# Performance work log

Hardware: AMD Instinct MI355X
Metric: run time of the kernel (lower is better)

The kernel has to match this reference:

```python
import jax, jax.numpy as jnp
import numpy as np

B, N, G, C = 4, 4000, 64, 91
H, W = 800.0, 1333.0
FG_THRESH, BG_THRESH = 0.5, 0.5
SCORE_THRESH, NMS_THRESH = 0.05, 0.5
DET_PER_IMG = 100
PRE_NMS_TOPK = 2048   # candidates entering NMS per image
MIN_SIZE = 0.01
BBOX_XFORM_CLIP = float(np.log(1000.0 / 16.0))
WX, WY, WW, WH = 10.0, 10.0, 5.0, 5.0  # bbox_reg_weights


def _rand_boxes(key, shape):
    k1, k2 = jax.random.split(key)
    xy = jax.random.uniform(k1, shape[:-1] + (2,)) * jnp.array([W * 0.8, H * 0.8], jnp.float32)
    wh = jax.random.uniform(k2, shape[:-1] + (2,)) * jnp.array([W * 0.2, H * 0.2], jnp.float32) + 2.0
    return jnp.concatenate([xy, xy + wh], axis=-1)


def setup_inputs():
    key = jax.random.key(0)
    ks = jax.random.split(key, 5)
    proposals = _rand_boxes(ks[0], (B, N, 4))
    gt_boxes = _rand_boxes(ks[1], (B, G, 4))
    gt_labels = jax.random.randint(ks[2], (B, G), 1, C)
    class_logits = jax.random.normal(ks[3], (B, N, C), dtype=jnp.float32)
    box_regression = jax.random.normal(ks[4], (B, N, C * 4), dtype=jnp.float32) * 0.1
    return {"proposals": proposals, "gt_boxes": gt_boxes, "gt_labels": gt_labels,
            "class_logits": class_logits, "box_regression": box_regression}


def box_iou(a, b):
    # a [A,4], b [B,4] -> [A,B]
    area_a = (a[:, 2] - a[:, 0]) * (a[:, 3] - a[:, 1])
    area_b = (b[:, 2] - b[:, 0]) * (b[:, 3] - b[:, 1])
    lt = jnp.maximum(a[:, None, :2], b[None, :, :2])
    rb = jnp.minimum(a[:, None, 2:], b[None, :, 2:])
    wh = jnp.clip(rb - lt, 0.0)
    inter = wh[..., 0] * wh[..., 1]
    return inter / (area_a[:, None] + area_b[None, :] - inter)


def encode(gt, prop):
    # BoxCoder.encode with weights (10,10,5,5)
    pw = prop[:, 2] - prop[:, 0]; ph = prop[:, 3] - prop[:, 1]
    px = prop[:, 0] + 0.5 * pw;  py = prop[:, 1] + 0.5 * ph
    gw = gt[:, 2] - gt[:, 0];    gh = gt[:, 3] - gt[:, 1]
    gx = gt[:, 0] + 0.5 * gw;    gy = gt[:, 1] + 0.5 * gh
    return jnp.stack([WX * (gx - px) / pw, WY * (gy - py) / ph,
                      WW * jnp.log(gw / pw), WH * jnp.log(gh / ph)], axis=1)


def decode(deltas, boxes):
    # deltas [N,C,4], boxes [N,4] -> [N,C,4]
    pw = boxes[:, 2] - boxes[:, 0]; ph = boxes[:, 3] - boxes[:, 1]
    px = boxes[:, 0] + 0.5 * pw;    py = boxes[:, 1] + 0.5 * ph
    dx = deltas[..., 0] / WX; dy = deltas[..., 1] / WY
    dw = jnp.minimum(deltas[..., 2] / WW, BBOX_XFORM_CLIP)
    dh = jnp.minimum(deltas[..., 3] / WH, BBOX_XFORM_CLIP)
    cx = dx * pw[:, None] + px[:, None]; cy = dy * ph[:, None] + py[:, None]
    w = jnp.exp(dw) * pw[:, None];       h = jnp.exp(dh) * ph[:, None]
    return jnp.stack([cx - 0.5 * w, cy - 0.5 * h, cx + 0.5 * w, cy + 0.5 * h], axis=-1)


def _image_fwd(prop, gt_b, gt_l, logits, regr):
    # --- assign_targets_to_proposals (with add_gt_proposals) ---
    props_all = jnp.concatenate([prop, gt_b], axis=0)          # [N+G,4]
    iou = box_iou(gt_b, props_all)                             # [G,N+G]
    matched_vals = iou.max(axis=0)
    matches = iou.argmax(axis=0)
    lbl = jnp.where(matched_vals >= FG_THRESH, gt_l[matches],
                    jnp.where(matched_vals < BG_THRESH, 0, -1))
    reg_targets = encode(gt_b[matches], props_all)             # [N+G,4]

    # --- postprocess_detections: decode + softmax + per-class NMS ---
    deltas = regr.reshape(N, C, 4)
    pb = decode(deltas, prop)                                  # [N,C,4]
    pb = jnp.stack([jnp.clip(pb[..., 0], 0.0, W), jnp.clip(pb[..., 1], 0.0, H),
                    jnp.clip(pb[..., 2], 0.0, W), jnp.clip(pb[..., 3], 0.0, H)], axis=-1)
    scores = jax.nn.softmax(logits, axis=-1)                   # [N,C]
    boxes_f = pb[:, 1:].reshape(-1, 4)                         # drop background class
    scores_f = scores[:, 1:].reshape(-1)
    labels_f = jnp.broadcast_to(jnp.arange(1, C), (N, C - 1)).reshape(-1)
    wf = boxes_f[:, 2] - boxes_f[:, 0]; hf = boxes_f[:, 3] - boxes_f[:, 1]
    valid = (scores_f > SCORE_THRESH) & (wf >= MIN_SIZE) & (hf >= MIN_SIZE)
    masked = jnp.where(valid, scores_f, -1.0)
    top_vals, top_idx = jax.lax.top_k(masked, PRE_NMS_TOPK)    # score-sorted candidates
    cb = boxes_f[top_idx]; cl = labels_f[top_idx]; cs = scores_f[top_idx]
    cv = top_vals > 0.0
    # batched_nms via per-class coordinate offset
    off = cl.astype(cb.dtype) * (max(W, H) + 1.0)
    ob = cb + off[:, None]
    iou_c = box_iou(ob, ob)                                    # [M,M]
    order = jnp.arange(PRE_NMS_TOPK)

    def body(i, keep):
        sup = keep[i] & (iou_c[i] > NMS_THRESH) & (order > i)
        return keep & ~sup

    keep = jax.lax.fori_loop(0, PRE_NMS_TOPK, body, cv)
    rank = jnp.cumsum(keep) - 1
    out_pos = jnp.where(keep & (rank < DET_PER_IMG), rank, DET_PER_IMG)  # OOB -> drop
    det_b = jnp.zeros((DET_PER_IMG, 4), cb.dtype).at[out_pos].set(cb, mode='drop')
    det_s = jnp.zeros((DET_PER_IMG,), cs.dtype).at[out_pos].set(cs, mode='drop')
    det_l = jnp.zeros((DET_PER_IMG,), cl.dtype).at[out_pos].set(cl, mode='drop')
    det = jnp.concatenate([det_b, det_s[:, None]], axis=-1)    # [K,5]
    return det, reg_targets, lbl, det_l


def reference(proposals, gt_boxes, gt_labels, class_logits, box_regression):
    return jax.vmap(_image_fwd)(proposals, gt_boxes, gt_labels, class_logits, box_regression)
```

## Files before the change

### kernel.cpp

```cpp
#include <hip/hip_runtime.h>
#include <cstdint>
#include <cstddef>

#define Bn   4
#define Nn   4000
#define Gn   64
#define Cn   91
#define FGC  90
#define NSEG 64
#define CAPSEG 256
#define CAPC (NSEG*CAPSEG)
#define SELCAP 4096
#define MSEL 2048
#define DETK 100

__device__ __constant__ float kW = 1333.0f;
__device__ __constant__ float kH = 800.0f;
#define XCLIP 4.135166556742356f
#define OFFMUL 1334.0f

#define NB 9216
#define SBIAS 0x3D400000u

typedef __attribute__((ext_vector_type(2))) unsigned long long u64x2;

#define OUT_DET  0
#define OUT_REG  (Bn*DETK*5)
#define OUT_LBL  (OUT_REG + Bn*(Nn+Gn)*4)
#define OUT_DETL (OUT_LBL + Bn*(Nn+Gn))

#define ZERO_N16 (148736/16)

__device__ __forceinline__ void decode_box(float4 p, float4 d,
                                           float& bx1, float& by1, float& bx2, float& by2) {
    float pw = p.z - p.x, ph = p.w - p.y;
    float px = p.x + 0.5f * pw, py = p.y + 0.5f * ph;
    float dx = d.x / 10.0f, dy = d.y / 10.0f;
    float dw = fminf(d.z / 5.0f, XCLIP), dh = fminf(d.w / 5.0f, XCLIP);
    float cx = dx * pw + px, cy = dy * ph + py;
    float w = expf(dw) * pw, h = expf(dh) * ph;
    bx1 = fminf(fmaxf(cx - 0.5f * w, 0.0f), kW);
    by1 = fminf(fmaxf(cy - 0.5f * h, 0.0f), kH);
    bx2 = fminf(fmaxf(cx + 0.5f * w, 0.0f), kW);
    by2 = fminf(fmaxf(cy + 0.5f * h, 0.0f), kH);
}

__device__ __forceinline__ unsigned score_bucket(unsigned sb) {
    unsigned h = (sb - SBIAS) >> 12;
    return h > (NB - 1) ? (NB - 1) : h;
}

__global__ __launch_bounds__(256) void zero_k(uint4* __restrict__ p) {
    int i = blockIdx.x * 256 + threadIdx.x;
    if (i < ZERO_N16) p[i] = make_uint4(0, 0, 0, 0);
}

__global__ __launch_bounds__(256) void fused_cand_k(const float* __restrict__ logits,
                                                    const float* __restrict__ regr,
                                                    const float* __restrict__ props,
                                                    unsigned long long* __restrict__ keys,
                                                    unsigned int* __restrict__ cnt,
                                                    unsigned int* __restrict__ hist) {
    int wave = threadIdx.x >> 6, lane = threadIdx.x & 63;
    int blk = blockIdx.x;
    int rowbase = blk * 16 + wave * 4;
    int b = blk / 250;
    int nbase = rowbase - b * Nn;
    bool has1 = (lane + 64) < Cn;
    const float* z = logits + (size_t)rowbase * Cn;
    float v0[4], v1[4], m[4], e[4];
    #pragma unroll
    for (int r = 0; r < 4; ++r) {
        v0[r] = z[r * Cn + lane];
        v1[r] = has1 ? z[r * Cn + lane + 64] : -INFINITY;
        m[r] = fmaxf(v0[r], v1[r]);
    }
    #pragma unroll
    for (int o = 32; o; o >>= 1) {
        #pragma unroll
        for (int r = 0; r < 4; ++r) m[r] = fmaxf(m[r], __shfl_xor(m[r], o));
    }
    #pragma unroll
    for (int r = 0; r < 4; ++r)
        e[r] = expf(v0[r] - m[r]) + (has1 ? expf(v1[r] - m[r]) : 0.0f);
    #pragma unroll
    for (int o = 32; o; o >>= 1) {
        #pragma unroll
        for (int r = 0; r < 4; ++r) e[r] += __shfl_xor(e[r], o);
    }
    unsigned long long keyA[4], keyB[4];
    bool vA[4], vB[4];
    #pragma unroll
    for (int r = 0; r < 4; ++r) {
        float s0 = expf(v0[r] - m[r]) / e[r];
        float s1 = has1 ? (expf(v1[r] - m[r]) / e[r]) : 0.0f;
        vA[r] = (lane >= 1) && (s0 > 0.05f);
        vB[r] = has1 && (s1 > 0.05f);
        keyA[r] = 0; keyB[r] = 0;
        float4 p = make_float4(0.f, 0.f, 0.f, 0.f);
        if (vA[r] || vB[r]) p = ((const float4*)props)[rowbase + r];
        if (vA[r]) {
            int c = lane;
            float4 d = ((const float4*)regr)[(size_t)(rowbase + r) * Cn + c];
            float bx1, by1, bx2, by2;
            decode_box(p, d, bx1, by1, bx2, by2);
            vA[r] = (bx2 - bx1 >= 0.01f) && (by2 - by1 >= 0.01f);
            unsigned idx = (unsigned)((nbase + r) * FGC + c - 1);
            keyA[r] = ((unsigned long long)__float_as_uint(s0) << 32) | (unsigned long long)(~idx);
            if (vA[r]) atomicAdd(&hist[b * NB + score_bucket(__float_as_uint(s0))], 1u);
        }
        if (vB[r]) {
            int c = lane + 64;
            float4 d = ((const float4*)regr)[(size_t)(rowbase + r) * Cn + c];
            float bx1, by1, bx2, by2;
            decode_box(p, d, bx1, by1, bx2, by2);
            vB[r] = (bx2 - bx1 >= 0.01f) && (by2 - by1 >= 0.01f);
            unsigned idx = (unsigned)((nbase + r) * FGC + c - 1);
            keyB[r] = ((unsigned long long)__float_as_uint(s1) << 32) | (unsigned long long)(~idx);
            if (vB[r]) atomicAdd(&hist[b * NB + score_bucket(__float_as_uint(s1))], 1u);
        }
    }
    unsigned long long mk[8];
    #pragma unroll
    for (int r = 0; r < 4; ++r) { mk[2*r] = __ballot(vA[r]); mk[2*r+1] = __ballot(vB[r]); }
    unsigned tot = 0, pre[8];
    #pragma unroll
    for (int q = 0; q < 8; ++q) { pre[q] = tot; tot += (unsigned)__popcll(mk[q]); }
    if (tot) {
        int seg = b * NSEG + (blk & (NSEG - 1));
        unsigned base = 0;
        if (lane == 0) base = atomicAdd(&cnt[seg], tot);
        base = __shfl(base, 0);
        unsigned long long lmask = (lane == 63) ? (~0ull >> 1) : ((1ull << lane) - 1);
        size_t segbase = (size_t)seg * CAPSEG;
        #pragma unroll
        for (int r = 0; r < 4; ++r) {
            if (vA[r]) {
                unsigned pos = base + pre[2*r] + (unsigned)__popcll(mk[2*r] & lmask);
                if (pos < CAPSEG) keys[segbase + pos] = keyA[r];
            }
            if (vB[r]) {
                unsigned pos = base + pre[2*r+1] + (unsigned)__popcll(mk[2*r+1] & lmask);
                if (pos < CAPSEG) keys[segbase + pos] = keyB[r];
            }
        }
    }
}

__global__ __launch_bounds__(256) void compact_k(const unsigned long long* __restrict__ keys,
                                                 const unsigned int* __restrict__ cnt,
                                                 const unsigned int* __restrict__ hist,
                                                 unsigned long long* __restrict__ sel,
                                                 unsigned int* __restrict__ cnt2) {
    int b = blockIdx.x >> 4, blk = blockIdx.x & 15;
    int tid = threadIdx.x, lane = tid & 63, wv = tid >> 6;
    __shared__ unsigned wtot[4], wt2[4], sscnt[NSEG];
    __shared__ unsigned sT, sbase;

    const uint4* h4 = (const uint4*)(hist + b * NB);
    unsigned hc[36]; unsigned s = 0;
    #pragma unroll
    for (int q = 0; q < 9; ++q) {
        uint4 t4 = h4[tid * 9 + q];
        hc[q*4+0] = t4.x; hc[q*4+1] = t4.y; hc[q*4+2] = t4.z; hc[q*4+3] = t4.w;
        s += t4.x + t4.y + t4.z + t4.w;
    }
    unsigned x = s;
    #pragma unroll
    for (int o = 1; o < 64; o <<= 1) { unsigned v = __shfl_down(x, o); if (lane + o < 64) x += v; }
    if (lane == 0) wtot[wv] = x;
    if (tid < NSEG) { unsigned c = cnt[b * NSEG + tid]; sscnt[tid] = c > CAPSEG ? CAPSEG : c; }
    __syncthreads();
    unsigned above = 0, total = 0;
    #pragma unroll
    for (int i2 = 0; i2 < 4; ++i2) { unsigned w2 = wtot[i2]; total += w2; if (i2 > wv) above += w2; }
    unsigned K2 = total < MSEL ? total : MSEL;
    if (K2 == 0) return;
    unsigned run = (x - s) + above;
    #pragma unroll
    for (int q = 35; q >= 0; --q) {
        unsigned c = hc[q], lo = run;
        run += c;
        if (lo < K2 && K2 <= run) sT = (unsigned)(tid * 36 + q);
    }
    __syncthreads();
    unsigned T = sT;

    unsigned long long k0 = 0, k1 = 0, k2 = 0, k3 = 0;
    bool v0 = false, v1 = false, v2 = false, v3 = false;
    {
        int g = blk * 1024 + 0 * 256 + tid; unsigned seg = g >> 8, ss = g & 255;
        if (ss < sscnt[seg]) { unsigned long long k = keys[(size_t)b * CAPC + g];
            if (score_bucket((unsigned)(k >> 32)) >= T) { k0 = k; v0 = true; } }
    }
    {
        int g = blk * 1024 + 1 * 256 + tid; unsigned seg = g >> 8, ss = g & 255;
        if (ss < sscnt[seg]) { unsigned long long k = keys[(size_t)b * CAPC + g];
            if (score_bucket((unsigned)(k >> 32)) >= T) { k1 = k; v1 = true; } }
    }
    {
        int g = blk * 1024 + 2 * 256 + tid; unsigned seg = g >> 8, ss = g & 255;
        if (ss < sscnt[seg]) { unsigned long long k = keys[(size_t)b * CAPC + g];
            if (score_bucket((unsigned)(k >> 32)) >= T) { k2 = k; v2 = true; } }
    }
    {
        int g = blk * 1024 + 3 * 256 + tid; unsigned seg = g >> 8, ss = g & 255;
        if (ss < sscnt[seg]) { unsigned long long k = keys[(size_t)b * CAPC + g];
            if (score_bucket((unsigned)(k >> 32)) >= T) { k3 = k; v3 = true; } }
    }
    unsigned c2 = (unsigned)v0 + (unsigned)v1 + (unsigned)v2 + (unsigned)v3;
    unsigned inc = c2;
    #pragma unroll
    for (int o = 1; o < 64; o <<= 1) { unsigned v = __shfl_up(inc, o); if (lane >= o) inc += v; }
    unsigned excl = inc - c2;
    if (lane == 63) wt2[wv] = inc;
    __syncthreads();
    if (tid == 0) {
        unsigned tot = wt2[0] + wt2[1] + wt2[2] + wt2[3];
        sbase = tot ? atomicAdd(&cnt2[b], tot) : 0u;
    }
    __syncthreads();
    unsigned pos = sbase + excl;
    #pragma unroll
    for (int i2 = 0; i2 < 4; ++i2) if (i2 < wv) pos += wt2[i2];
    unsigned long long* selb = sel + (size_t)b * SELCAP;
    unsigned q0 = pos, q1 = q0 + v0, q2 = q1 + v1, q3 = q2 + v2;
    if (v0 && q0 < SELCAP) selb[q0] = k0;
    if (v1 && q1 < SELCAP) selb[q1] = k1;
    if (v2 && q2 < SELCAP) selb[q2] = k2;
    if (v3 && q3 < SELCAP) selb[q3] = k3;
}

__global__ __launch_bounds__(256) void rank_k(const unsigned long long* __restrict__ sel,
                                              const unsigned int* __restrict__ cnt2,
                                              unsigned long long* __restrict__ selkeys) {
    int b = blockIdx.x >> 6, blk = blockIdx.x & 63;
    unsigned n2 = cnt2[b]; if (n2 > SELCAP) n2 = SELCAP;
    if ((unsigned)(blk * 64) >= n2) return;
    int lane = threadIdx.x & 63, wv = threadIdx.x >> 6;
    int sub = blk * 64 + lane;
    __shared__ __align__(16) unsigned long long skk[SELCAP + 2];
    __shared__ unsigned pc[4][64];
    unsigned n2p = (n2 + 1) & ~1u;
    const unsigned long long* selb = sel + (size_t)b * SELCAP;
    for (unsigned s2 = threadIdx.x; s2 < n2p; s2 += 256)
        skk[s2] = (s2 < n2) ? selb[s2] : 0ull;
    __syncthreads();
    unsigned long long mk = (sub < (int)n2) ? skk[sub] : ~0ull;
    bool act = (sub < (int)n2) && ((mk >> 32) != 0ull);
    unsigned pairs = n2p >> 1;
    unsigned Q = (pairs + 3) >> 2;
    unsigned jb = wv * Q, je = jb + Q; if (je > pairs) je = pairs;
    const u64x2* sk2 = (const u64x2*)skk;
    unsigned cntg = 0;
    for (unsigned j = jb; j < je; ++j) {
        u64x2 kk = sk2[j];
        cntg += (unsigned)(kk.x > mk) + (unsigned)(kk.y > mk);
    }
    pc[wv][lane] = cntg;
    __syncthreads();
    if (wv == 0) {
        unsigned rank = pc[0][lane] + pc[1][lane] + pc[2][lane] + pc[3][lane];
        if (act && rank < MSEL) selkeys[(size_t)b * MSEL + rank] = mk;
    }
}

__global__ __launch_bounds__(256) void select_k(const unsigned long long* __restrict__ selkeys,
                                                const unsigned int* __restrict__ cnt2,
                                                const float* __restrict__ props,
                                                const float* __restrict__ regr,
                                                float* __restrict__ cb, float* __restrict__ ob,
                                                float* __restrict__ sc, int* __restrict__ lab,
                                                unsigned long long* __restrict__ cvw) {
    int t = blockIdx.x * 256 + threadIdx.x;
    if (t >= Bn * MSEL) return;
    int b = t >> 11;
    unsigned n2 = cnt2[b]; if (n2 > SELCAP) n2 = SELCAP;
    unsigned validN = n2 < MSEL ? n2 : MSEL;
    unsigned slotrank = (unsigned)(t & (MSEL - 1));
    unsigned long long key = (slotrank < validN) ? selkeys[t] : 0ull;
    float bx1 = 0, by1 = 0, bx2 = 0, by2 = 0, score = 0;
    int c = 0; unsigned valid = 0;
    if ((key >> 32) != 0ull) {
        valid = 1;
        unsigned idx = ~(unsigned)key;
        int n = idx / FGC, cm1 = idx - n * FGC;
        c = cm1 + 1;
        score = __uint_as_float((unsigned)(key >> 32));
        int row = b * Nn + n;
        float4 p = ((const float4*)props)[row];
        float4 d = ((const float4*)regr)[(size_t)row * Cn + c];
        decode_box(p, d, bx1, by1, bx2, by2);
    }
    float off = (float)c * OFFMUL;
    cb[t * 4 + 0] = bx1; cb[t * 4 + 1] = by1; cb[t * 4 + 2] = bx2; cb[t * 4 + 3] = by2;
    ob[t * 4 + 0] = bx1 + off; ob[t * 4 + 1] = by1 + off;
    ob[t * 4 + 2] = bx2 + off; ob[t * 4 + 3] = by2 + off;
    sc[t] = score; lab[t] = c;
    unsigned long long bw = __ballot(valid != 0u);
    if ((t & 63) == 0) cvw[t >> 6] = bw;
}

__global__ __launch_bounds__(256) void nmsmat_k(const float* __restrict__ ob,
                                                unsigned long long* __restrict__ M) {
    int blk = blockIdx.x;
    int b = blk >> 8, rc = (blk >> 5) & 7, w = blk & 31;
    int i = rc * 256 + threadIdx.x;
    size_t mi = ((size_t)b * MSEL + i) * 32 + w;
    if (w * 64 + 63 <= rc * 256) {
        M[mi] = 0ull;
        return;
    }
    __shared__ float4 sj[64];
    const float4* obf4 = (const float4*)(ob + (size_t)b * MSEL * 4);
    if (threadIdx.x < 64) sj[threadIdx.x] = obf4[w * 64 + threadIdx.x];
    __syncthreads();
    float4 bi = obf4[i];
    float areai = (bi.z - bi.x) * (bi.w - bi.y);
    unsigned long long bits = 0ull;
    #pragma unroll 16
    for (int tt = 0; tt < 64; ++tt) {
        int j = w * 64 + tt;
        float4 bj = sj[tt];
        float xx1 = fmaxf(bi.x, bj.x), yy1 = fmaxf(bi.y, bj.y);
        float xx2 = fminf(bi.z, bj.z), yy2 = fminf(bi.w, bj.w);
        float iw = fmaxf(xx2 - xx1, 0.0f), ih = fmaxf(yy2 - yy1, 0.0f);
        float inter = iw * ih;
        float areaj = (bj.z - bj.x) * (bj.w - bj.y);
        float iou = inter / (areai + areaj - inter);
        if ((iou > 0.5f) && (j > i)) bits |= (1ull << tt);
    }
    M[mi] = bits;
}

__global__ __launch_bounds__(64) void scan_k(const unsigned long long* __restrict__ M,
                                             const unsigned long long* __restrict__ cvw,
                                             const float* __restrict__ cb,
                                             const float* __restrict__ sc,
                                             const int* __restrict__ lab,
                                             float* __restrict__ out) {
    int b = blockIdx.x, lane = threadIdx.x;
    const bool ld = lane < 32;
    unsigned long long keep = ld ? cvw[b * 32 + lane] : 0ull;
    unsigned kLo = (unsigned)keep, kHi = (unsigned)(keep >> 32);
    __shared__ int keptIdx[DETK];
    const unsigned long long* Mb = M + (size_t)b * MSEL * 32;
    int kcount = 0;
    unsigned long long Abuf[16], Bbuf[16];
    #pragma unroll
    for (int k = 0; k < 16; ++k) Abuf[k] = ld ? Mb[(size_t)k * 32 + lane] : 0ull;
    for (int g = 0; g < 128; g += 2) {
        #pragma unroll
        for (int k = 0; k < 16; ++k)
            Bbuf[k] = ld ? Mb[(size_t)((g + 1) * 16 + k) * 32 + lane] : 0ull;
        {
            int base = g * 16;
            int rl = base >> 6, sh = base & 31;
            unsigned half = (base >> 5) & 1;
            #pragma unroll
            for (int k = 0; k < 16; ++k) {
                unsigned kw = half ? kHi : kLo;
                unsigned bitv = (__builtin_amdgcn_readlane(kw, rl) >> (sh + k)) & 1u;
                if (bitv) {
                    unsigned long long m = Abuf[k];
                    kLo &= ~(unsigned)m; kHi &= ~(unsigned)(m >> 32);
                    if (kcount < DETK && lane == 0) keptIdx[kcount] = base + k;
                    ++kcount;
                }
            }
        }
        if (kcount >= DETK) break;
        if (g + 2 < 128) {
            #pragma unroll
            for (int k = 0; k < 16; ++k)
                Abuf[k] = ld ? Mb[(size_t)((g + 2) * 16 + k) * 32 + lane] : 0ull;
        }
        {
            int base = (g + 1) * 16;
            int rl = base >> 6, sh = base & 31;
            unsigned half = (base >> 5) & 1;
            #pragma unroll
            for (int k = 0; k < 16; ++k) {
                unsigned kw = half ? kHi : kLo;
                unsigned bitv = (__builtin_amdgcn_readlane(kw, rl) >> (sh + k)) & 1u;
                if (bitv) {
                    unsigned long long m = Bbuf[k];
                    kLo &= ~(unsigned)m; kHi &= ~(unsigned)(m >> 32);
                    if (kcount < DETK && lane == 0) keptIdx[kcount] = base + k;
                    ++kcount;
                }
            }
        }
        if (kcount >= DETK) break;
    }
    __syncthreads();
    int kept100 = kcount < DETK ? kcount : DETK;
    for (int r = lane; r < kept100; r += 64) {
        int i = keptIdx[r];
        int slot = b * MSEL + i;
        float* dr = out + OUT_DET + ((size_t)b * DETK + r) * 5;
        dr[0] = cb[slot * 4 + 0]; dr[1] = cb[slot * 4 + 1];
        dr[2] = cb[slot * 4 + 2]; dr[3] = cb[slot * 4 + 3];
        dr[4] = sc[slot];
        out[OUT_DETL + b * DETK + r] = (float)lab[slot];
    }
    for (int r = kept100 + lane; r < DETK; r += 64) {
        float* dr = out + OUT_DET + ((size_t)b * DETK + r) * 5;
        dr[0] = dr[1] = dr[2] = dr[3] = dr[4] = 0.0f;
        out[OUT_DETL + b * DETK + r] = 0.0f;
    }
}

__global__ __launch_bounds__(256) void assign_k(const float* __restrict__ props,
                                                const float* __restrict__ gtb,
                                                const int* __restrict__ gtl,
                                                float* __restrict__ out) {
    __shared__ float4 sg[Gn];
    int b = blockIdx.y;
    int p = blockIdx.x * 256 + threadIdx.x;
    if (threadIdx.x < Gn) sg[threadIdx.x] = ((const float4*)(gtb + (size_t)b * Gn * 4))[threadIdx.x];
    __syncthreads();
    if (p >= Nn + Gn) return;
    float4 pb = (p < Nn) ? ((const float4*)(props + (size_t)b * Nn * 4))[p] : sg[p - Nn];
    float areap = (pb.z - pb.x) * (pb.w - pb.y);
    float best = -1.0f; int bi = 0;
    #pragma unroll 4
    for (int g = 0; g < Gn; ++g) {
        float4 gb = sg[g];
        float xx1 = fmaxf(gb.x, pb.x), yy1 = fmaxf(gb.y, pb.y);
        float xx2 = fminf(gb.z, pb.z), yy2 = fminf(gb.w, pb.w);
        float iw = fmaxf(xx2 - xx1, 0.0f), ih = fmaxf(yy2 - yy1, 0.0f);
        float inter = iw * ih;
        float areag = (gb.z - gb.x) * (gb.w - gb.y);
        float iou = inter / (areag + areap - inter);
        if (iou > best) { best = iou; bi = g; }
    }
    float4 gb = sg[bi];
    float pw = pb.z - pb.x, ph = pb.w - pb.y;
    float px = pb.x + 0.5f * pw, py = pb.y + 0.5f * ph;
    float gw = gb.z - gb.x, gh = gb.w - gb.y;
    float gx = gb.x + 0.5f * gw, gy = gb.y + 0.5f * gh;
    float* rr = out + OUT_REG + ((size_t)b * (Nn + Gn) + p) * 4;
    rr[0] = 10.0f * (gx - px) / pw;
    rr[1] = 10.0f * (gy - py) / ph;
    rr[2] = 5.0f * logf(gw / pw);
    rr[3] = 5.0f * logf(gh / ph);
    out[OUT_LBL + (size_t)b * (Nn + Gn) + p] = (best >= 0.5f) ? (float)gtl[b * Gn + bi] : 0.0f;
}

extern "C" void kernel_launch(void* const* d_in, const int* in_sizes, int n_in,
                              void* d_out, int out_size, void* d_ws, size_t ws_size,
                              hipStream_t stream) {
    const float* props  = (const float*)d_in[0];
    const float* gtb    = (const float*)d_in[1];
    const int*   gtl    = (const int*)d_in[2];
    const float* logits = (const float*)d_in[3];
    const float* regr   = (const float*)d_in[4];
    float* out = (float*)d_out;

    char* w = (char*)d_ws;
    unsigned int* cnt           = (unsigned int*)(w + 0);
    unsigned int* cnt2          = (unsigned int*)(w + 1024);
    unsigned int* hist          = (unsigned int*)(w + 1280);
    unsigned long long* sel     = (unsigned long long*)(w + 148736);
    unsigned long long* selkeys = (unsigned long long*)(w + 279808);
    unsigned long long* keys    = (unsigned long long*)(w + 345344);
    float* cb                   = (float*)(w + 869632);
    float* ob                   = (float*)(w + 1000704);
    float* sc                   = (float*)(w + 1131776);
    int* lab                    = (int*)(w + 1164544);
    unsigned long long* cvw     = (unsigned long long*)(w + 1197312);
    unsigned long long* M       = (unsigned long long*)(w + 1198336);
    (void)ws_size; (void)in_sizes; (void)n_in; (void)out_size;

    zero_k<<<(ZERO_N16 + 255) / 256, 256, 0, stream>>>((uint4*)w);
    fused_cand_k<<<Bn * Nn / 16, 256, 0, stream>>>(logits, regr, props, keys, cnt, hist);
    compact_k<<<Bn * 16, 256, 0, stream>>>(keys, cnt, hist, sel, cnt2);
    rank_k<<<Bn * 64, 256, 0, stream>>>(sel, cnt2, selkeys);
    select_k<<<(Bn * MSEL) / 256, 256, 0, stream>>>(selkeys, cnt2, props, regr, cb, ob, sc, lab, cvw);
    nmsmat_k<<<Bn * 256, 256, 0, stream>>>(ob, M);
    scan_k<<<Bn, 64, 0, stream>>>(M, cvw, cb, sc, lab, out);
    assign_k<<<dim3((Nn + Gn + 255) / 256, Bn), 256, 0, stream>>>(props, gtb, gtl, out);
}
```

Baseline: 87.77 us.

## Restructure candidate pipeline: per-block slots, shared-memory histogram, fused rank-select

Each candidate block now holds 32 rows and owns a fixed key slot range. Its count goes to a shared-memory counter that is written out at the end, so the separate zeroing kernel is no longer needed. The global atomic score histogram moves into compact_k, now one block per image, which builds the histogram in shared memory from the stored keys. The rank and select kernels are fused so decode happens right at the ranked position. The valid-bit array is dropped because scan_k derives the keep mask from the selected count. Two launches go away, but compaction now runs on only four blocks and loops serially over 20000 slots each.

Result: slower. 112.0 us (+27.6%).

```diff
diff --git a/kernel.cpp b/kernel.cpp
--- a/kernel.cpp
+++ b/kernel.cpp
@@ -7,9 +7,11 @@
 #define Gn   64
 #define Cn   91
 #define FGC  90
-#define NSEG 64
-#define CAPSEG 256
-#define CAPC (NSEG*CAPSEG)
+#define RPW  8
+#define BLKROWS 32
+#define NBLKI 125
+#define CAPSEG 160
+#define SLOTSI (NBLKI*CAPSEG)
 #define SELCAP 4096
 #define MSEL 2048
 #define DETK 100
@@ -28,8 +30,6 @@
 #define OUT_REG  (Bn*DETK*5)
 #define OUT_LBL  (OUT_REG + Bn*(Nn+Gn)*4)
 #define OUT_DETL (OUT_LBL + Bn*(Nn+Gn))
-
-#define ZERO_N16 (148736/16)
 
 __device__ __forceinline__ void decode_box(float4 p, float4 d,
                                            float& bx1, float& by1, float& bx2, float& by2) {
@@ -50,27 +50,23 @@
     return h > (NB - 1) ? (NB - 1) : h;
 }
 
-__global__ __launch_bounds__(256) void zero_k(uint4* __restrict__ p) {
-    int i = blockIdx.x * 256 + threadIdx.x;
-    if (i < ZERO_N16) p[i] = make_uint4(0, 0, 0, 0);
-}
-
 __global__ __launch_bounds__(256) void fused_cand_k(const float* __restrict__ logits,
                                                     const float* __restrict__ regr,
                                                     const float* __restrict__ props,
                                                     unsigned long long* __restrict__ keys,
-                                                    unsigned int* __restrict__ cnt,
-                                                    unsigned int* __restrict__ hist) {
+                                                    unsigned int* __restrict__ cnt) {
+    __shared__ unsigned lcnt;
     int wave = threadIdx.x >> 6, lane = threadIdx.x & 63;
     int blk = blockIdx.x;
-    int rowbase = blk * 16 + wave * 4;
-    int b = blk / 250;
+    if (threadIdx.x == 0) lcnt = 0;
+    int rowbase = blk * BLKROWS + wave * RPW;
+    int b = blk / NBLKI;
     int nbase = rowbase - b * Nn;
     bool has1 = (lane + 64) < Cn;
     const float* z = logits + (size_t)rowbase * Cn;
-    float v0[4], v1[4], m[4], e[4];
-    #pragma unroll
-    for (int r = 0; r < 4; ++r) {
+    float v0[RPW], v1[RPW], m[RPW], e[RPW], t0[RPW], t1[RPW];
+    #pragma unroll
+    for (int r = 0; r < RPW; ++r) {
         v0[r] = z[r * Cn + lane];
         v1[r] = has1 ? z[r * Cn + lane + 64] : -INFINITY;
         m[r] = fmaxf(v0[r], v1[r]);
@@ -78,22 +74,25 @@
     #pragma unroll
     for (int o = 32; o; o >>= 1) {
         #pragma unroll
-        for (int r = 0; r < 4; ++r) m[r] = fmaxf(m[r], __shfl_xor(m[r], o));
-    }
-    #pragma unroll
-    for (int r = 0; r < 4; ++r)
-        e[r] = expf(v0[r] - m[r]) + (has1 ? expf(v1[r] - m[r]) : 0.0f);
+        for (int r = 0; r < RPW; ++r) m[r] = fmaxf(m[r], __shfl_xor(m[r], o));
+    }
+    #pragma unroll
+    for (int r = 0; r < RPW; ++r) {
+        t0[r] = expf(v0[r] - m[r]);
+        t1[r] = has1 ? expf(v1[r] - m[r]) : 0.0f;
+        e[r] = t0[r] + t1[r];
+    }
     #pragma unroll
     for (int o = 32; o; o >>= 1) {
         #pragma unroll
-        for (int r = 0; r < 4; ++r) e[r] += __shfl_xor(e[r], o);
-    }
-    unsigned long long keyA[4], keyB[4];
-    bool vA[4], vB[4];
-    #pragma unroll
-    for (int r = 0; r < 4; ++r) {
-        float s0 = expf(v0[r] - m[r]) / e[r];
-        float s1 = has1 ? (expf(v1[r] - m[r]) / e[r]) : 0.0f;
+        for (int r = 0; r < RPW; ++r) e[r] += __shfl_xor(e[r], o);
+    }
+    unsigned long long keyA[RPW], keyB[RPW];
+    bool vA[RPW], vB[RPW];
+    #pragma unroll
+    for (int r = 0; r < RPW; ++r) {
+        float s0 = t0[r] / e[r];
+        float s1 = has1 ? (t1[r] / e[r]) : 0.0f;
         vA[r] = (lane >= 1) && (s0 > 0.05f);
         vB[r] = has1 && (s1 > 0.05f);
         keyA[r] = 0; keyB[r] = 0;
@@ -107,7 +106,6 @@
             vA[r] = (bx2 - bx1 >= 0.01f) && (by2 - by1 >= 0.01f);
             unsigned idx = (unsigned)((nbase + r) * FGC + c - 1);
             keyA[r] = ((unsigned long long)__float_as_uint(s0) << 32) | (unsigned long long)(~idx);
-            if (vA[r]) atomicAdd(&hist[b * NB + score_bucket(__float_as_uint(s0))], 1u);
         }
         if (vB[r]) {
             int c = lane + 64;
@@ -117,24 +115,23 @@
             vB[r] = (bx2 - bx1 >= 0.01f) && (by2 - by1 >= 0.01f);
             unsigned idx = (unsigned)((nbase + r) * FGC + c - 1);
             keyB[r] = ((unsigned long long)__float_as_uint(s1) << 32) | (unsigned long long)(~idx);
-            if (vB[r]) atomicAdd(&hist[b * NB + score_bucket(__float_as_uint(s1))], 1u);
-        }
-    }
-    unsigned long long mk[8];
-    #pragma unroll
-    for (int r = 0; r < 4; ++r) { mk[2*r] = __ballot(vA[r]); mk[2*r+1] = __ballot(vB[r]); }
-    unsigned tot = 0, pre[8];
-    #pragma unroll
-    for (int q = 0; q < 8; ++q) { pre[q] = tot; tot += (unsigned)__popcll(mk[q]); }
+        }
+    }
+    __syncthreads();
+    unsigned long long mk[2 * RPW];
+    #pragma unroll
+    for (int r = 0; r < RPW; ++r) { mk[2*r] = __ballot(vA[r]); mk[2*r+1] = __ballot(vB[r]); }
+    unsigned tot = 0, pre[2 * RPW];
+    #pragma unroll
+    for (int q = 0; q < 2 * RPW; ++q) { pre[q] = tot; tot += (unsigned)__popcll(mk[q]); }
     if (tot) {
-        int seg = b * NSEG + (blk & (NSEG - 1));
         unsigned base = 0;
-        if (lane == 0) base = atomicAdd(&cnt[seg], tot);
+        if (lane == 0) base = atomicAdd(&lcnt, tot);
         base = __shfl(base, 0);
         unsigned long long lmask = (lane == 63) ? (~0ull >> 1) : ((1ull << lane) - 1);
-        size_t segbase = (size_t)seg * CAPSEG;
+        size_t segbase = (size_t)blk * CAPSEG;
         #pragma unroll
-        for (int r = 0; r < 4; ++r) {
+        for (int r = 0; r < RPW; ++r) {
             if (vA[r]) {
                 unsigned pos = base + pre[2*r] + (unsigned)__popcll(mk[2*r] & lmask);
                 if (pos < CAPSEG) keys[segbase + pos] = keyA[r];
@@ -145,95 +142,76 @@
             }
         }
     }
+    __syncthreads();
+    if (threadIdx.x == 0) cnt[blk] = lcnt;
 }
 
 __global__ __launch_bounds__(256) void compact_k(const unsigned long long* __restrict__ keys,
                                                  const unsigned int* __restrict__ cnt,
-                                                 const unsigned int* __restrict__ hist,
                                                  unsigned long long* __restrict__ sel,
                                                  unsigned int* __restrict__ cnt2) {
-    int b = blockIdx.x >> 4, blk = blockIdx.x & 15;
-    int tid = threadIdx.x, lane = tid & 63, wv = tid >> 6;
-    __shared__ unsigned wtot[4], wt2[4], sscnt[NSEG];
-    __shared__ unsigned sT, sbase;
-
-    const uint4* h4 = (const uint4*)(hist + b * NB);
-    unsigned hc[36]; unsigned s = 0;
-    #pragma unroll
-    for (int q = 0; q < 9; ++q) {
-        uint4 t4 = h4[tid * 9 + q];
-        hc[q*4+0] = t4.x; hc[q*4+1] = t4.y; hc[q*4+2] = t4.z; hc[q*4+3] = t4.w;
-        s += t4.x + t4.y + t4.z + t4.w;
-    }
-    unsigned x = s;
+    __shared__ unsigned hist[NB];
+    __shared__ unsigned sscnt[NBLKI];
+    __shared__ unsigned wtot[4];
+    __shared__ unsigned sT, lsel;
+    int b = blockIdx.x, tid = threadIdx.x, lane = tid & 63, wv = tid >> 6;
+    for (int h = tid; h < NB; h += 256) hist[h] = 0;
+    if (tid < NBLKI) { unsigned c = cnt[b * NBLKI + tid]; sscnt[tid] = c > CAPSEG ? CAPSEG : c; }
+    if (tid == 0) { sT = NB; lsel = 0; }
+    __syncthreads();
+    const unsigned long long* kb = keys + (size_t)b * SLOTSI;
+    for (int g = tid; g < SLOTSI; g += 256) {
+        int seg = g / CAPSEG, s = g - seg * CAPSEG;
+        if (s < (int)sscnt[seg])
+            atomicAdd(&hist[score_bucket((unsigned)(kb[g] >> 32))], 1u);
+    }
+    __syncthreads();
+    unsigned hc[36]; unsigned ssum = 0;
+    #pragma unroll
+    for (int q = 0; q < 36; ++q) { hc[q] = hist[tid * 36 + q]; ssum += hc[q]; }
+    unsigned x = ssum;
     #pragma unroll
     for (int o = 1; o < 64; o <<= 1) { unsigned v = __shfl_down(x, o); if (lane + o < 64) x += v; }
     if (lane == 0) wtot[wv] = x;
-    if (tid < NSEG) { unsigned c = cnt[b * NSEG + tid]; sscnt[tid] = c > CAPSEG ? CAPSEG : c; }
     __syncthreads();
     unsigned above = 0, total = 0;
     #pragma unroll
     for (int i2 = 0; i2 < 4; ++i2) { unsigned w2 = wtot[i2]; total += w2; if (i2 > wv) above += w2; }
     unsigned K2 = total < MSEL ? total : MSEL;
-    if (K2 == 0) return;
-    unsigned run = (x - s) + above;
-    #pragma unroll
-    for (int q = 35; q >= 0; --q) {
-        unsigned c = hc[q], lo = run;
-        run += c;
-        if (lo < K2 && K2 <= run) sT = (unsigned)(tid * 36 + q);
+    if (K2) {
+        unsigned run = (x - ssum) + above;
+        #pragma unroll
+        for (int q = 35; q >= 0; --q) {
+            unsigned c = hc[q], lo = run;
+            run += c;
+            if (lo < K2 && K2 <= run) sT = (unsigned)(tid * 36 + q);
+        }
     }
     __syncthreads();
     unsigned T = sT;
-
-    unsigned long long k0 = 0, k1 = 0, k2 = 0, k3 = 0;
-    bool v0 = false, v1 = false, v2 = false, v3 = false;
-    {
-        int g = blk * 1024 + 0 * 256 + tid; unsigned seg = g >> 8, ss = g & 255;
-        if (ss < sscnt[seg]) { unsigned long long k = keys[(size_t)b * CAPC + g];
-            if (score_bucket((unsigned)(k >> 32)) >= T) { k0 = k; v0 = true; } }
-    }
-    {
-        int g = blk * 1024 + 1 * 256 + tid; unsigned seg = g >> 8, ss = g & 255;
-        if (ss < sscnt[seg]) { unsigned long long k = keys[(size_t)b * CAPC + g];
-            if (score_bucket((unsigned)(k >> 32)) >= T) { k1 = k; v1 = true; } }
-    }
-    {
-        int g = blk * 1024 + 2 * 256 + tid; unsigned seg = g >> 8, ss = g & 255;
-        if (ss < sscnt[seg]) { unsigned long long k = keys[(size_t)b * CAPC + g];
-            if (score_bucket((unsigned)(k >> 32)) >= T) { k2 = k; v2 = true; } }
-    }
-    {
-        int g = blk * 1024 + 3 * 256 + tid; unsigned seg = g >> 8, ss = g & 255;
-        if (ss < sscnt[seg]) { unsigned long long k = keys[(size_t)b * CAPC + g];
-            if (score_bucket((unsigned)(k >> 32)) >= T) { k3 = k; v3 = true; } }
-    }
-    unsigned c2 = (unsigned)v0 + (unsigned)v1 + (unsigned)v2 + (unsigned)v3;
-    unsigned inc = c2;
-    #pragma unroll
-    for (int o = 1; o < 64; o <<= 1) { unsigned v = __shfl_up(inc, o); if (lane >= o) inc += v; }
-    unsigned excl = inc - c2;
-    if (lane == 63) wt2[wv] = inc;
-    __syncthreads();
-    if (tid == 0) {
-        unsigned tot = wt2[0] + wt2[1] + wt2[2] + wt2[3];
-        sbase = tot ? atomicAdd(&cnt2[b], tot) : 0u;
-    }
-    __syncthreads();
-    unsigned pos = sbase + excl;
-    #pragma unroll
-    for (int i2 = 0; i2 < 4; ++i2) if (i2 < wv) pos += wt2[i2];
-    unsigned long long* selb = sel + (size_t)b * SELCAP;
-    unsigned q0 = pos, q1 = q0 + v0, q2 = q1 + v1, q3 = q2 + v2;
-    if (v0 && q0 < SELCAP) selb[q0] = k0;
-    if (v1 && q1 < SELCAP) selb[q1] = k1;
-    if (v2 && q2 < SELCAP) selb[q2] = k2;
-    if (v3 && q3 < SELCAP) selb[q3] = k3;
-}
-
-__global__ __launch_bounds__(256) void rank_k(const unsigned long long* __restrict__ sel,
-                                              const unsigned int* __restrict__ cnt2,
-                                              unsigned long long* __restrict__ selkeys) {
+    if (K2) {
+        unsigned long long* selb = sel + (size_t)b * SELCAP;
+        for (int g = tid; g < SLOTSI; g += 256) {
+            int seg = g / CAPSEG, s = g - seg * CAPSEG;
+            if (s < (int)sscnt[seg]) {
+                unsigned long long k = kb[g];
+                if (score_bucket((unsigned)(k >> 32)) >= T) {
+                    unsigned pos = atomicAdd(&lsel, 1u);
+                    if (pos < SELCAP) selb[pos] = k;
+                }
+            }
+        }
+    }
+    __syncthreads();
+    if (tid == 0) cnt2[b] = lsel;
+}
+
+__global__ __launch_bounds__(256) void rank_sel_k(const unsigned long long* __restrict__ sel,
+                                                  const unsigned int* __restrict__ cnt2,
+                                                  const float* __restrict__ props,
+                                                  const float* __restrict__ regr,
+                                                  float* __restrict__ cb, float* __restrict__ ob,
+                                                  float* __restrict__ sc, int* __restrict__ lab) {
     int b = blockIdx.x >> 6, blk = blockIdx.x & 63;
     unsigned n2 = cnt2[b]; if (n2 > SELCAP) n2 = SELCAP;
     if ((unsigned)(blk * 64) >= n2) return;
@@ -261,44 +239,24 @@
     __syncthreads();
     if (wv == 0) {
         unsigned rank = pc[0][lane] + pc[1][lane] + pc[2][lane] + pc[3][lane];
-        if (act && rank < MSEL) selkeys[(size_t)b * MSEL + rank] = mk;
-    }
-}
-
-__global__ __launch_bounds__(256) void select_k(const unsigned long long* __restrict__ selkeys,
-                                                const unsigned int* __restrict__ cnt2,
-                                                const float* __restrict__ props,
-                                                const float* __restrict__ regr,
-                                                float* __restrict__ cb, float* __restrict__ ob,
-                                                float* __restrict__ sc, int* __restrict__ lab,
-                                                unsigned long long* __restrict__ cvw) {
-    int t = blockIdx.x * 256 + threadIdx.x;
-    if (t >= Bn * MSEL) return;
-    int b = t >> 11;
-    unsigned n2 = cnt2[b]; if (n2 > SELCAP) n2 = SELCAP;
-    unsigned validN = n2 < MSEL ? n2 : MSEL;
-    unsigned slotrank = (unsigned)(t & (MSEL - 1));
-    unsigned long long key = (slotrank < validN) ? selkeys[t] : 0ull;
-    float bx1 = 0, by1 = 0, bx2 = 0, by2 = 0, score = 0;
-    int c = 0; unsigned valid = 0;
-    if ((key >> 32) != 0ull) {
-        valid = 1;
-        unsigned idx = ~(unsigned)key;
-        int n = idx / FGC, cm1 = idx - n * FGC;
-        c = cm1 + 1;
-        score = __uint_as_float((unsigned)(key >> 32));
-        int row = b * Nn + n;
-        float4 p = ((const float4*)props)[row];
-        float4 d = ((const float4*)regr)[(size_t)row * Cn + c];
-        decode_box(p, d, bx1, by1, bx2, by2);
-    }
-    float off = (float)c * OFFMUL;
-    cb[t * 4 + 0] = bx1; cb[t * 4 + 1] = by1; cb[t * 4 + 2] = bx2; cb[t * 4 + 3] = by2;
-    ob[t * 4 + 0] = bx1 + off; ob[t * 4 + 1] = by1 + off;
-    ob[t * 4 + 2] = bx2 + off; ob[t * 4 + 3] = by2 + off;
-    sc[t] = score; lab[t] = c;
-    unsigned long long bw = __ballot(valid != 0u);
-    if ((t & 63) == 0) cvw[t >> 6] = bw;
+        if (act && rank < MSEL) {
+            int t = b * MSEL + (int)rank;
+            unsigned idx = ~(unsigned)mk;
+            int n = idx / FGC, cm1 = idx - n * FGC;
+            int c = cm1 + 1;
+            float score = __uint_as_float((unsigned)(mk >> 32));
+            int row = b * Nn + n;
+            float4 p = ((const float4*)props)[row];
+            float4 d = ((const float4*)regr)[(size_t)row * Cn + c];
+            float bx1, by1, bx2, by2;
+            decode_box(p, d, bx1, by1, bx2, by2);
+            float off = (float)c * OFFMUL;
+            cb[t * 4 + 0] = bx1; cb[t * 4 + 1] = by1; cb[t * 4 + 2] = bx2; cb[t * 4 + 3] = by2;
+            ob[t * 4 + 0] = bx1 + off; ob[t * 4 + 1] = by1 + off;
+            ob[t * 4 + 2] = bx2 + off; ob[t * 4 + 3] = by2 + off;
+            sc[t] = score; lab[t] = c;
+        }
+    }
 }
 
 __global__ __launch_bounds__(256) void nmsmat_k(const float* __restrict__ ob,
@@ -334,14 +292,21 @@
 }
 
 __global__ __launch_bounds__(64) void scan_k(const unsigned long long* __restrict__ M,
-                                             const unsigned long long* __restrict__ cvw,
+                                             const unsigned int* __restrict__ cnt2,
                                              const float* __restrict__ cb,
                                              const float* __restrict__ sc,
                                              const int* __restrict__ lab,
                                              float* __restrict__ out) {
     int b = blockIdx.x, lane = threadIdx.x;
     const bool ld = lane < 32;
-    unsigned long long keep = ld ? cvw[b * 32 + lane] : 0ull;
+    unsigned n2 = cnt2[b]; if (n2 > SELCAP) n2 = SELCAP;
+    int validN = (int)(n2 < MSEL ? n2 : MSEL);
+    unsigned long long keep = 0ull;
+    if (ld) {
+        int base = lane * 64;
+        keep = (base + 64 <= validN) ? ~0ull
+             : (base >= validN ? 0ull : ((1ull << (validN - base)) - 1ull));
+    }
     unsigned kLo = (unsigned)keep, kHi = (unsigned)(keep >> 32);
     __shared__ int keptIdx[DETK];
     const unsigned long long* Mb = M + (size_t)b * MSEL * 32;
@@ -460,25 +425,20 @@
 
     char* w = (char*)d_ws;
     unsigned int* cnt           = (unsigned int*)(w + 0);
-    unsigned int* cnt2          = (unsigned int*)(w + 1024);
-    unsigned int* hist          = (unsigned int*)(w + 1280);
-    unsigned long long* sel     = (unsigned long long*)(w + 148736);
-    unsigned long long* selkeys = (unsigned long long*)(w + 279808);
-    unsigned long long* keys    = (unsigned long long*)(w + 345344);
-    float* cb                   = (float*)(w + 869632);
-    float* ob                   = (float*)(w + 1000704);
-    float* sc                   = (float*)(w + 1131776);
-    int* lab                    = (int*)(w + 1164544);
-    unsigned long long* cvw     = (unsigned long long*)(w + 1197312);
-    unsigned long long* M       = (unsigned long long*)(w + 1198336);
+    unsigned int* cnt2          = (unsigned int*)(w + 2048);
+    unsigned long long* sel     = (unsigned long long*)(w + 2304);
+    unsigned long long* keys    = (unsigned long long*)(w + 133376);
+    float* cb                   = (float*)(w + 773376);
+    float* ob                   = (float*)(w + 904448);
+    float* sc                   = (float*)(w + 1035520);
+    int* lab                    = (int*)(w + 1068288);
+    unsigned long long* M       = (unsigned long long*)(w + 1101056);
     (void)ws_size; (void)in_sizes; (void)n_in; (void)out_size;
 
-    zero_k<<<(ZERO_N16 + 255) / 256, 256, 0, stream>>>((uint4*)w);
-    fused_cand_k<<<Bn * Nn / 16, 256, 0, stream>>>(logits, regr, props, keys, cnt, hist);
-    compact_k<<<Bn * 16, 256, 0, stream>>>(keys, cnt, hist, sel, cnt2);
-    rank_k<<<Bn * 64, 256, 0, stream>>>(sel, cnt2, selkeys);
-    select_k<<<(Bn * MSEL) / 256, 256, 0, stream>>>(selkeys, cnt2, props, regr, cb, ob, sc, lab, cvw);
+    fused_cand_k<<<Bn * NBLKI, 256, 0, stream>>>(logits, regr, props, keys, cnt);
+    compact_k<<<Bn, 256, 0, stream>>>(keys, cnt, sel, cnt2);
+    rank_sel_k<<<Bn * 64, 256, 0, stream>>>(sel, cnt2, props, regr, cb, ob, sc, lab);
     nmsmat_k<<<Bn * 256, 256, 0, stream>>>(ob, M);
-    scan_k<<<Bn, 64, 0, stream>>>(M, cvw, cb, sc, lab, out);
+    scan_k<<<Bn, 64, 0, stream>>>(M, cnt2, cb, sc, lab, out);
     assign_k<<<dim3((Nn + Gn + 255) / 256, Bn), 256, 0, stream>>>(props, gtb, gtl, out);
 }
```
